# Optimization experiments

Hardware: AMD Instinct MI355X
Metric: run time of the kernel (lower is better)

## Reference

```python
import jax, jax.numpy as jnp
import numpy as np

B, K, V = 128, 8, 50257   # batch, beam_size, num_syms
L, MAXL = 64, 128         # current cand seq length, max_seq_len
A, D = 512, 1024          # attention_dim, decoder_dim
EOS = 2
NEG = -1.0e9


def setup_inputs() -> dict:
    key = jax.random.key(0)
    ks = jax.random.split(key, 9)
    return {
        "logits": jax.random.normal(ks[0], (B, K, V), dtype=jnp.float32),
        "cand_scores": jax.random.normal(ks[1], (B, K), dtype=jnp.float32),
        "cand_seqs": jax.random.randint(ks[2], (B, K, L), 0, V, dtype=jnp.int32),
        "completed_scores": jax.random.normal(ks[3], (B, K), dtype=jnp.float32),
        "completed_seqs": jax.random.randint(ks[4], (B, K, MAXL), 0, V, dtype=jnp.int32),
        "completed_length": jax.random.randint(ks[5], (B, K), 1, MAXL, dtype=jnp.int32),
        "decoder_context": jax.random.normal(ks[6], (B * K, A), dtype=jnp.float32),
        "decoder_rnn1": jax.random.normal(ks[7], (B * K, D), dtype=jnp.float32),
        "decoder_rnn2": jax.random.normal(ks[8], (B * K, D), dtype=jnp.float32),
    }


def reference(logits, cand_scores, cand_seqs, completed_scores, completed_seqs,
              completed_length, decoder_context, decoder_rnn1, decoder_rnn2):
    # --- beam_search_score: normalize logits, accumulate path scores ---
    logprobs = jax.nn.log_softmax(logits, axis=2)            # [B,K,V]
    new_scores = logprobs + cand_scores[:, :, None]          # [B,K,V]

    # --- deal_with_completed: append eos-terminated hyps, length-normalized top-k ---
    eos_scores = new_scores[:, :, EOS]                                   # [B,K]
    comp_scores = jnp.concatenate([completed_scores, eos_scores], 1)     # [B,2K]
    eos_tail = jnp.full((B, K, MAXL - L), EOS, dtype=cand_seqs.dtype)
    new_comp_seqs = jnp.concatenate([cand_seqs, eos_tail], 2)            # [B,K,MAXL]
    comp_seqs = jnp.concatenate([completed_seqs, new_comp_seqs], 1)      # [B,2K,MAXL]
    comp_len = jnp.concatenate(
        [completed_length, jnp.full((B, K), L + 1, dtype=completed_length.dtype)], 1)
    rescaled = comp_scores / comp_len.astype(comp_scores.dtype)
    _, cinds = jax.lax.top_k(rescaled, K)                                # [B,K]
    comp_scores = jnp.take_along_axis(comp_scores, cinds, axis=1)
    comp_seqs = jnp.take_along_axis(comp_seqs, cinds[:, :, None], axis=1)
    comp_len = jnp.take_along_axis(comp_len, cinds, axis=1)

    # --- deal_with_uncompleted: top-k over beam*vocab excluding eos ---
    masked = new_scores.at[:, :, EOS].set(NEG)
    flat = masked.reshape(B, K * V)
    new_cand_scores, inds = jax.lax.top_k(flat, K)                       # [B,K]
    parents = inds // V                                                  # [B,K]
    syms = (inds % V).astype(cand_seqs.dtype)
    new_seqs = jnp.take_along_axis(cand_seqs, parents[:, :, None], axis=1)
    new_seqs = jnp.concatenate([new_seqs, syms[:, :, None]], axis=2)     # [B,K,L+1]

    # reorder decoder states by parent beam index
    pidx = parents[:, :, None]
    ctx = jnp.take_along_axis(decoder_context.reshape(B, K, A), pidx, axis=1).reshape(-1, A)
    r1 = jnp.take_along_axis(decoder_rnn1.reshape(B, K, D), pidx, axis=1).reshape(-1, D)
    r2 = jnp.take_along_axis(decoder_rnn2.reshape(B, K, D), pidx, axis=1).reshape(-1, D)

    return (new_cand_scores, new_seqs, parents, comp_scores, comp_seqs, comp_len, ctx, r1, r2)
```

## Files before the change

kernel.cpp:

```cpp
#include <hip/hip_runtime.h>


#define BB 128
#define KK 8
#define VV 50257
#define LL 64
#define MAXLEN 128
#define AA 512
#define DD 1024
#define EOSI 2
#define NTHR 256

constexpr size_t O0 = 0;
constexpr size_t O1 = 1024;
constexpr size_t O2 = 67584;
constexpr size_t O3 = 68608;
constexpr size_t O4 = 69632;
constexpr size_t O5 = 200704;
constexpr size_t O6 = 201728;
constexpr size_t O7 = 726016;
constexpr size_t O8 = 1774592;

__device__ __forceinline__ bool better(float v2, int i2, float v1, int i1) {
  return (v2 > v1) || (v2 == v1 && i2 < i1);
}

__global__ __launch_bounds__(NTHR) void k_rowpass(
    const float* __restrict__ logits,
    float* __restrict__ ws_max, float* __restrict__ ws_lse,
    float* __restrict__ ws_eos,
    float* __restrict__ ws_tv, int* __restrict__ ws_ti) {
  const int r = blockIdx.x;
  const int tid = threadIdx.x;
  const float* __restrict__ row = logits + (size_t)r * VV;
  if (tid == 0) ws_eos[r] = row[EOSI];

  float m = -INFINITY, s = 0.0f;
  float tv[8]; int ti[8];
#pragma unroll
  for (int i = 0; i < 8; ++i) { tv[i] = -INFINITY; ti[i] = 0x7fffffff; }

  auto proc = [&](float px, int pi) {
    if (px > m) { s = s * __expf(m - px) + 1.0f; m = px; }
    else        { s += __expf(px - m); }
    if (pi != EOSI && better(px, pi, tv[7], ti[7])) {
      tv[7] = px; ti[7] = pi;
#pragma unroll
      for (int jj = 7; jj > 0; --jj) {
        if (better(tv[jj], ti[jj], tv[jj - 1], ti[jj - 1])) {
          float tf = tv[jj]; tv[jj] = tv[jj - 1]; tv[jj - 1] = tf;
          int tq = ti[jj]; ti[jj] = ti[jj - 1]; ti[jj - 1] = tq;
        }
      }
    }
  };

  const int pre = (4 - (r & 3)) & 3;
  const int nvec = (VV - pre) >> 2;
  const int rem = VV - pre - (nvec << 2);
  if (tid < pre) proc(row[tid], tid);
  if (tid >= 8 && tid < 8 + rem) {
    int e = pre + (nvec << 2) + (tid - 8);
    proc(row[e], e);
  }
  const float4* __restrict__ vrow = (const float4*)(row + pre);
  for (int i = tid; i < nvec; i += NTHR) {
    float4 x = vrow[i];
    int i0 = pre + (i << 2);
    proc(x.x, i0);
    proc(x.y, i0 + 1);
    proc(x.z, i0 + 2);
    proc(x.w, i0 + 3);
  }

  const int lane = tid & 63;
  const int wid = tid >> 6;

  for (int off = 32; off; off >>= 1) {
    float m2 = __shfl_down(m, off);
    float s2 = __shfl_down(s, off);
    float M = fmaxf(m, m2);
    s = s * __expf(m - M) + s2 * __expf(m2 - M);
    m = M;
  }
  __shared__ float shm[4], shs[4];
  __shared__ float lv[NTHR * 8];
  __shared__ int   li[NTHR * 8];
  __shared__ float rv4[4]; __shared__ int ri4[4], rl4[4];
  if (lane == 0) { shm[wid] = m; shs[wid] = s; }
#pragma unroll
  for (int i = 0; i < 8; ++i) { lv[i * NTHR + tid] = tv[i]; li[i * NTHR + tid] = ti[i]; }
  __syncthreads();
  if (tid == 0) {
    float M = shm[0], S = shs[0];
    for (int w = 1; w < 4; ++w) {
      float M2 = fmaxf(M, shm[w]);
      S = S * __expf(M - M2) + shs[w] * __expf(shm[w] - M2);
      M = M2;
    }
    ws_max[r] = M;
    ws_lse[r] = logf(S);
  }
  for (int sel = 0; sel < 8; ++sel) {
    float bv = -INFINITY; int bi = 0x7fffffff; int bl = -1;
#pragma unroll
    for (int j = 0; j < 8; ++j) {
      int p = j * NTHR + tid;
      if (better(lv[p], li[p], bv, bi)) { bv = lv[p]; bi = li[p]; bl = p; }
    }
    for (int off = 32; off; off >>= 1) {
      float v2 = __shfl_down(bv, off);
      int i2 = __shfl_down(bi, off);
      int l2 = __shfl_down(bl, off);
      if (better(v2, i2, bv, bi)) { bv = v2; bi = i2; bl = l2; }
    }
    if (lane == 0) { rv4[wid] = bv; ri4[wid] = bi; rl4[wid] = bl; }
    __syncthreads();
    if (tid == 0) {
      float fv = rv4[0]; int fi = ri4[0], fl = rl4[0];
      for (int w = 1; w < 4; ++w)
        if (better(rv4[w], ri4[w], fv, fi)) { fv = rv4[w]; fi = ri4[w]; fl = rl4[w]; }
      ws_tv[r * 8 + sel] = fv;
      ws_ti[r * 8 + sel] = fi;
      lv[fl] = -INFINITY; li[fl] = 0x7fffffff;
    }
    __syncthreads();
  }
}

__global__ __launch_bounds__(NTHR) void k_select(
    const float* __restrict__ cand_scores, const int* __restrict__ cand_seqs,
    const float* __restrict__ completed_scores, const int* __restrict__ completed_seqs,
    const int* __restrict__ completed_length,
    const float* __restrict__ ws_max, const float* __restrict__ ws_lse,
    const float* __restrict__ ws_eos, const float* __restrict__ ws_tv,
    const int* __restrict__ ws_ti, int* __restrict__ ws_par,
    float* __restrict__ out) {
  const int b = blockIdx.x;
  const int tid = threadIdx.x;
  __shared__ float sh_mx[KK], sh_lse[KK], sh_cand[KK];
  __shared__ float sh_ncs[KK]; __shared__ int sh_par[KK], sh_sym[KK];
  __shared__ float sh_cs[KK];  __shared__ int sh_clen[KK], sh_cind[KK];
  if (tid < KK) {
    sh_mx[tid] = ws_max[b * KK + tid];
    sh_lse[tid] = ws_lse[b * KK + tid];
    sh_cand[tid] = cand_scores[b * KK + tid];
  }
  __syncthreads();
  if (tid < 64) {
    const int lane = tid;
    const int k = lane >> 3, j = lane & 7;
    float x = ws_tv[(b * KK + k) * 8 + j];
    int v = ws_ti[(b * KK + k) * 8 + j];
    float val = ((x - sh_mx[k]) - sh_lse[k]) + sh_cand[k];
    int flat = k * VV + v;
    if (v == 0x7fffffff) { val = -INFINITY; flat = 0x7fffffff; }
    for (int sel = 0; sel < 8; ++sel) {
      float bv = val; int bi = flat; int bl = lane;
      for (int off = 32; off; off >>= 1) {
        float v2 = __shfl_down(bv, off);
        int i2 = __shfl_down(bi, off);
        int l2 = __shfl_down(bl, off);
        if (better(v2, i2, bv, bi)) { bv = v2; bi = i2; bl = l2; }
      }
      int wl = __shfl(bl, 0);
      if (lane == wl) {
        sh_ncs[sel] = val; sh_par[sel] = flat / VV; sh_sym[sel] = flat % VV;
        val = -INFINITY; flat = 0x7fffffff;
      }
    }
    float cs; int clen;
    if (lane < KK) {
      cs = completed_scores[b * KK + lane];
      clen = completed_length[b * KK + lane];
    } else if (lane < 2 * KK) {
      int k2 = lane - KK;
      cs = ((ws_eos[b * KK + k2] - sh_mx[k2]) - sh_lse[k2]) + sh_cand[k2];
      clen = LL + 1;
    } else { cs = -INFINITY; clen = 1; }
    float rsc = (lane < 2 * KK) ? cs / (float)clen : -INFINITY;
    for (int sel = 0; sel < 8; ++sel) {
      float bv = rsc; int bi = lane;
      for (int off = 32; off; off >>= 1) {
        float v2 = __shfl_down(bv, off);
        int i2 = __shfl_down(bi, off);
        if (better(v2, i2, bv, bi)) { bv = v2; bi = i2; }
      }
      int wl = __shfl(bi, 0);
      if (lane == wl) {
        sh_cs[sel] = cs; sh_clen[sel] = clen; sh_cind[sel] = lane;
        rsc = -INFINITY;
      }
    }
  }
  __syncthreads();
  if (tid < KK) {
    out[O0 + (size_t)b * KK + tid] = sh_ncs[tid];
    out[O2 + (size_t)b * KK + tid] = (float)sh_par[tid];
    out[O3 + (size_t)b * KK + tid] = sh_cs[tid];
    out[O5 + (size_t)b * KK + tid] = (float)sh_clen[tid];
    ws_par[b * KK + tid] = sh_par[tid];
  }
  for (int t = tid; t < KK * (LL + 1); t += NTHR) {
    int i = t / (LL + 1), pos = t - i * (LL + 1);
    int val;
    if (pos < LL) val = cand_seqs[((size_t)b * KK + sh_par[i]) * LL + pos];
    else val = sh_sym[i];
    out[O1 + ((size_t)b * KK + i) * (LL + 1) + pos] = (float)val;
  }
  for (int t = tid; t < KK * MAXLEN; t += NTHR) {
    int i = t >> 7, pos = t & 127;
    int c = sh_cind[i];
    int val;
    if (c < KK) val = completed_seqs[((size_t)b * KK + c) * MAXLEN + pos];
    else {
      int k2 = c - KK;
      val = (pos < LL) ? cand_seqs[((size_t)b * KK + k2) * LL + pos] : EOSI;
    }
    out[O4 + ((size_t)b * KK + i) * MAXLEN + pos] = (float)val;
  }
}

__global__ __launch_bounds__(NTHR) void k_gather(
    const float* __restrict__ ctx, const float* __restrict__ r1,
    const float* __restrict__ r2, const int* __restrict__ ws_par,
    float* __restrict__ out) {
  const int r = blockIdx.x;
  const int b = r >> 3;
  const int src = (b << 3) + ws_par[r];
  const int tid = threadIdx.x;
  {
    const float4* s4 = (const float4*)(ctx + (size_t)src * AA);
    float4* d4 = (float4*)(out + O6 + (size_t)r * AA);
    for (int i = tid; i < AA / 4; i += NTHR) d4[i] = s4[i];
  }
  {
    const float4* s4 = (const float4*)(r1 + (size_t)src * DD);
    float4* d4 = (float4*)(out + O7 + (size_t)r * DD);
    for (int i = tid; i < DD / 4; i += NTHR) d4[i] = s4[i];
  }
  {
    const float4* s4 = (const float4*)(r2 + (size_t)src * DD);
    float4* d4 = (float4*)(out + O8 + (size_t)r * DD);
    for (int i = tid; i < DD / 4; i += NTHR) d4[i] = s4[i];
  }
}

extern "C" void kernel_launch(void* const* d_in, const int* in_sizes, int n_in,
                              void* d_out, int out_size, void* d_ws, size_t ws_size,
                              hipStream_t stream) {
  const float* logits = (const float*)d_in[0];
  const float* cand_scores = (const float*)d_in[1];
  const int* cand_seqs = (const int*)d_in[2];
  const float* completed_scores = (const float*)d_in[3];
  const int* completed_seqs = (const int*)d_in[4];
  const int* completed_length = (const int*)d_in[5];
  const float* dctx = (const float*)d_in[6];
  const float* drnn1 = (const float*)d_in[7];
  const float* drnn2 = (const float*)d_in[8];
  float* out = (float*)d_out;

  float* ws_max = (float*)d_ws;
  float* ws_lse = ws_max + BB * KK;
  float* ws_eos = ws_lse + BB * KK;
  float* ws_tv = ws_eos + BB * KK;
  int* ws_ti = (int*)(ws_tv + BB * KK * 8);
  int* ws_par = ws_ti + BB * KK * 8;

  k_rowpass<<<BB * KK, NTHR, 0, stream>>>(logits, ws_max, ws_lse, ws_eos, ws_tv, ws_ti);
  k_select<<<BB, NTHR, 0, stream>>>(cand_scores, cand_seqs, completed_scores,
                                    completed_seqs, completed_length, ws_max, ws_lse,
                                    ws_eos, ws_tv, ws_ti, ws_par, out);
  k_gather<<<BB * KK, NTHR, 0, stream>>>(dctx, drnn1, drnn2, ws_par, out);
}
```

Baseline: 370.2 us.

## Replace per-thread top-8 insertion with threshold filtering and unshifted exp-sum

```diff
diff --git a/kernel.cpp b/kernel.cpp
--- a/kernel.cpp
+++ b/kernel.cpp
@@ -10,6 +10,7 @@
 #define DD 1024
 #define EOSI 2
 #define NTHR 256
+#define CAP 2048
 
 constexpr size_t O0 = 0;
 constexpr size_t O1 = 1024;
@@ -32,81 +33,103 @@
     float* __restrict__ ws_tv, int* __restrict__ ws_ti) {
   const int r = blockIdx.x;
   const int tid = threadIdx.x;
+  const int lane = tid & 63, wid = tid >> 6;
   const float* __restrict__ row = logits + (size_t)r * VV;
-  if (tid == 0) ws_eos[r] = row[EOSI];
-
-  float m = -INFINITY, s = 0.0f;
-  float tv[8]; int ti[8];
-#pragma unroll
-  for (int i = 0; i < 8; ++i) { tv[i] = -INFINITY; ti[i] = 0x7fffffff; }
-
-  auto proc = [&](float px, int pi) {
-    if (px > m) { s = s * __expf(m - px) + 1.0f; m = px; }
-    else        { s += __expf(px - m); }
-    if (pi != EOSI && better(px, pi, tv[7], ti[7])) {
-      tv[7] = px; ti[7] = pi;
-#pragma unroll
-      for (int jj = 7; jj > 0; --jj) {
-        if (better(tv[jj], ti[jj], tv[jj - 1], ti[jj - 1])) {
-          float tf = tv[jj]; tv[jj] = tv[jj - 1]; tv[jj - 1] = tf;
-          int tq = ti[jj]; ti[jj] = ti[jj - 1]; ti[jj - 1] = tq;
-        }
-      }
-    }
-  };
+
+  __shared__ float sm[NTHR];
+  __shared__ float red[8];
+  __shared__ float stau;
+  __shared__ int scnt;
+  __shared__ float cv[CAP];
+  __shared__ int ci[CAP];
+  __shared__ float rv4[4]; __shared__ int ri4[4], rl4[4];
+
+  if (tid == 0) { ws_eos[r] = row[EOSI]; scnt = 0; }
 
   const int pre = (4 - (r & 3)) & 3;
   const int nvec = (VV - pre) >> 2;
   const int rem = VV - pre - (nvec << 2);
-  if (tid < pre) proc(row[tid], tid);
+  const float4* __restrict__ vrow = (const float4*)(row + pre);
+
+  float m = -INFINITY, s0 = 0.0f, s1 = 0.0f;
+  if (tid < pre) { float x = row[tid]; s0 += __expf(x); m = fmaxf(m, x); }
+  if (tid >= 8 && tid < 8 + rem) {
+    float x = row[pre + (nvec << 2) + (tid - 8)];
+    s0 += __expf(x); m = fmaxf(m, x);
+  }
+  for (int i = tid; i < nvec; i += NTHR) {
+    float4 x = vrow[i];
+    s0 += __expf(x.x); s1 += __expf(x.y);
+    s0 += __expf(x.z); s1 += __expf(x.w);
+    m = fmaxf(fmaxf(x.x, x.y), m);
+    m = fmaxf(fmaxf(x.z, x.w), m);
+  }
+  float s = s0 + s1;
+  sm[tid] = m;
+  float mr = m;
+  for (int off = 32; off; off >>= 1) {
+    s += __shfl_down(s, off);
+    mr = fmaxf(mr, __shfl_down(mr, off));
+  }
+  if (lane == 0) { red[wid] = s; red[4 + wid] = mr; }
+  __syncthreads();
+  if (tid == 0) {
+    float S = (red[0] + red[1]) + (red[2] + red[3]);
+    float M = fmaxf(fmaxf(red[4], red[5]), fmaxf(red[6], red[7]));
+    ws_max[r] = M;
+    ws_lse[r] = logf(S) - M;
+  }
+
+  if (wid == 0) {
+    float v0 = sm[lane], v1 = sm[lane + 64], v2 = sm[lane + 128], v3 = sm[lane + 192];
+    float tau = -INFINITY;
+    for (int rr = 0; rr < 9; ++rr) {
+      float lm = fmaxf(fmaxf(v0, v1), fmaxf(v2, v3));
+      float wm = lm;
+      for (int off = 32; off; off >>= 1) wm = fmaxf(wm, __shfl_down(wm, off));
+      wm = __shfl(wm, 0);
+      tau = wm;
+      unsigned long long msk = __ballot(lm == wm);
+      int first = __ffsll((unsigned long long)msk) - 1;
+      if (lane == first) {
+        if (v0 == wm) v0 = -INFINITY;
+        else if (v1 == wm) v1 = -INFINITY;
+        else if (v2 == wm) v2 = -INFINITY;
+        else v3 = -INFINITY;
+      }
+    }
+    if (lane == 0) stau = tau;
+  }
+  __syncthreads();
+  const float tau = stau;
+
+  if (tid < pre) {
+    float x = row[tid];
+    if (x >= tau) { int p = atomicAdd(&scnt, 1); if (p < CAP) { cv[p] = x; ci[p] = tid; } }
+  }
   if (tid >= 8 && tid < 8 + rem) {
     int e = pre + (nvec << 2) + (tid - 8);
-    proc(row[e], e);
-  }
-  const float4* __restrict__ vrow = (const float4*)(row + pre);
+    float x = row[e];
+    if (x >= tau) { int p = atomicAdd(&scnt, 1); if (p < CAP) { cv[p] = x; ci[p] = e; } }
+  }
   for (int i = tid; i < nvec; i += NTHR) {
     float4 x = vrow[i];
-    int i0 = pre + (i << 2);
-    proc(x.x, i0);
-    proc(x.y, i0 + 1);
-    proc(x.z, i0 + 2);
-    proc(x.w, i0 + 3);
-  }
-
-  const int lane = tid & 63;
-  const int wid = tid >> 6;
-
-  for (int off = 32; off; off >>= 1) {
-    float m2 = __shfl_down(m, off);
-    float s2 = __shfl_down(s, off);
-    float M = fmaxf(m, m2);
-    s = s * __expf(m - M) + s2 * __expf(m2 - M);
-    m = M;
-  }
-  __shared__ float shm[4], shs[4];
-  __shared__ float lv[NTHR * 8];
-  __shared__ int   li[NTHR * 8];
-  __shared__ float rv4[4]; __shared__ int ri4[4], rl4[4];
-  if (lane == 0) { shm[wid] = m; shs[wid] = s; }
-#pragma unroll
-  for (int i = 0; i < 8; ++i) { lv[i * NTHR + tid] = tv[i]; li[i * NTHR + tid] = ti[i]; }
-  __syncthreads();
-  if (tid == 0) {
-    float M = shm[0], S = shs[0];
-    for (int w = 1; w < 4; ++w) {
-      float M2 = fmaxf(M, shm[w]);
-      S = S * __expf(M - M2) + shs[w] * __expf(shm[w] - M2);
-      M = M2;
-    }
-    ws_max[r] = M;
-    ws_lse[r] = logf(S);
-  }
+    if (x.x >= tau || x.y >= tau || x.z >= tau || x.w >= tau) {
+      int i0 = pre + (i << 2);
+      if (x.x >= tau) { int p = atomicAdd(&scnt, 1); if (p < CAP) { cv[p] = x.x; ci[p] = i0; } }
+      if (x.y >= tau) { int p = atomicAdd(&scnt, 1); if (p < CAP) { cv[p] = x.y; ci[p] = i0 + 1; } }
+      if (x.z >= tau) { int p = atomicAdd(&scnt, 1); if (p < CAP) { cv[p] = x.z; ci[p] = i0 + 2; } }
+      if (x.w >= tau) { int p = atomicAdd(&scnt, 1); if (p < CAP) { cv[p] = x.w; ci[p] = i0 + 3; } }
+    }
+  }
+  __syncthreads();
+
+  int n = scnt < CAP ? scnt : CAP;
   for (int sel = 0; sel < 8; ++sel) {
     float bv = -INFINITY; int bi = 0x7fffffff; int bl = -1;
-#pragma unroll
-    for (int j = 0; j < 8; ++j) {
-      int p = j * NTHR + tid;
-      if (better(lv[p], li[p], bv, bi)) { bv = lv[p]; bi = li[p]; bl = p; }
+    for (int j = tid; j < n; j += NTHR) {
+      float v = cv[j]; int idx = ci[j];
+      if (idx != EOSI && better(v, idx, bv, bi)) { bv = v; bi = idx; bl = j; }
     }
     for (int off = 32; off; off >>= 1) {
       float v2 = __shfl_down(bv, off);
@@ -122,7 +145,7 @@
         if (better(rv4[w], ri4[w], fv, fi)) { fv = rv4[w]; fi = ri4[w]; fl = rl4[w]; }
       ws_tv[r * 8 + sel] = fv;
       ws_ti[r * 8 + sel] = fi;
-      lv[fl] = -INFINITY; li[fl] = 0x7fffffff;
+      if (fl >= 0) cv[fl] = -INFINITY;
     }
     __syncthreads();
   }
```

Measured after the change: 357.4 us. 3.5% less time.
